# Kernel optimization log

Hardware: AMD Instinct MI355X
Metric: run time of the kernel (lower is better)

The kernel has to match this reference:

```python
import jax, jax.numpy as jnp
import numpy as np

N_SP = 32  # number of superpixels, hardcoded in the original module


def setup_inputs() -> dict:
    key = jax.random.key(0)
    k1, k2 = jax.random.split(key)
    b, c, h, w = 16, 64, 512, 512
    features = jax.random.normal(k1, (b, c, h, w), dtype=jnp.float32)
    superpixel_indices = jax.random.randint(k2, (b, h, w), 0, N_SP, dtype=jnp.int32)
    return {"features": features, "superpixel_indices": superpixel_indices}


def reference(features, superpixel_indices):
    b, c, h, w = features.shape
    # [b, h*w, c]
    feats = jnp.transpose(features, (0, 2, 3, 1)).reshape(b * h * w, c)
    # offset segment ids so all batches reduce in one segment_sum pass
    ids = (superpixel_indices.reshape(b, h * w)
           + (jnp.arange(b, dtype=superpixel_indices.dtype)[:, None] * N_SP)).reshape(-1)
    sums = jax.ops.segment_sum(feats, ids, num_segments=b * N_SP)          # [b*N, c]
    counts = jax.ops.segment_sum(jnp.ones((b * h * w,), feats.dtype), ids,
                                 num_segments=b * N_SP)                     # [b*N]
    # mean per superpixel; empty superpixels stay zero (matches torch init)
    sp = jnp.where(counts[:, None] > 0,
                   sums / jnp.maximum(counts[:, None], 1.0),
                   0.0).reshape(b, N_SP, c)
    # pairwise: sim[i,j] = 1 - 0.5 * ||sp_i - sp_j||^2  (N=32, tiny)
    diff = sp[:, :, None, :] - sp[:, None, :, :]        # [b, N, N, c]
    sim = 1.0 - 0.5 * jnp.sum(diff * diff, axis=-1)     # [b, N, N]
    return sp, sim
```

## Files before the change

### kernel.cpp

```cpp
#include <hip/hip_runtime.h>

#define NSP 32
#define BB  16
#define CC  64
#define HW  (512 * 512)

#define BLOCK  128
#define CHUNK  4096
#define NCHUNK (HW / CHUNK)
#define KIT    (CHUNK / 4 / BLOCK)
#define STR    (NSP + 1)
#define NGRP   (BLOCK / 32)

#define BAR() asm volatile("s_waitcnt lgkmcnt(0)\n\ts_barrier" ::: "memory")

__global__ __launch_bounds__(BLOCK) void sp_accum(const float* __restrict__ feats,
                                                  const int*   __restrict__ spidx,
                                                  float*       __restrict__ sums  ,
                                                  float*       __restrict__ counts)
{
    __shared__ float2 s_priv[BLOCK][STR];
    __shared__ float2 s_pe[NGRP][NSP];
    __shared__ float2 s_po[NGRP][NSP];

    const int tid  = threadIdx.x;
    const int b    = blockIdx.y;
    const int pix0 = blockIdx.x * CHUNK;
    const int bin  = tid & 31;
    const int grp  = tid >> 5;

    float2* row = s_priv[tid];

    uchar4 uu[KIT];
    {
        const int4* ip = (const int4*)(spidx + (size_t)b * HW + pix0);
#pragma unroll
        for (int k = 0; k < KIT; ++k) {
            int4 v = ip[k * BLOCK + tid];
            uu[k] = make_uchar4((unsigned char)(v.x & 31), (unsigned char)(v.y & 31),
                                (unsigned char)(v.z & 31), (unsigned char)(v.w & 31));
        }
    }
#pragma unroll
    for (int s = 0; s < STR; ++s) row[s] = make_float2(0.f, 0.f);

    const float* fb = feats + (size_t)b * CC * HW + pix0;
    float4 pre[KIT][2];
#pragma unroll
    for (int k = 0; k < KIT; ++k) {
        pre[k][0] = ((const float4*)fb)[k * BLOCK + tid];
        pre[k][1] = ((const float4*)(fb + (size_t)HW))[k * BLOCK + tid];
    }

#pragma unroll
    for (int k = 0; k < KIT; ++k) {
        row[uu[k].x].x += 1.f;
        row[uu[k].y].x += 1.f;
        row[uu[k].z].x += 1.f;
        row[uu[k].w].x += 1.f;
    }
    BAR();
    {
        float a = 0.f;
#pragma unroll
        for (int m = 0; m < BLOCK / NGRP; ++m) a += s_priv[grp + m * NGRP][bin].x;
        s_pe[grp][bin].x = a;
    }
    BAR();
#pragma unroll
    for (int s = 0; s < STR; ++s) row[s] = make_float2(0.f, 0.f);
    if (tid < NSP) {
        float r = 0.f;
#pragma unroll
        for (int g = 0; g < NGRP; ++g) r += s_pe[g][tid].x;
        atomicAdd(&counts[b * NSP + tid], r);
    }

    for (int p = 0; p < CC / 2; ++p) {
        const int ch0 = 2 * p;
        float2 (*part)[NSP] = (p & 1) ? s_po : s_pe;

#pragma unroll
        for (int k = 0; k < KIT; ++k) {
            const uchar4 u = uu[k];
            const float4 a = pre[k][0], c = pre[k][1];
            float2 t;
            t = row[u.x]; t.x += a.x; t.y += c.x; row[u.x] = t;
            t = row[u.y]; t.x += a.y; t.y += c.y; row[u.y] = t;
            t = row[u.z]; t.x += a.z; t.y += c.z; row[u.z] = t;
            t = row[u.w]; t.x += a.w; t.y += c.w; row[u.w] = t;
        }
        if (p + 1 < CC / 2) {
            const float* g0 = fb + (size_t)(ch0 + 2) * HW;
#pragma unroll
            for (int k = 0; k < KIT; ++k) {
                pre[k][0] = ((const float4*)g0)[k * BLOCK + tid];
                pre[k][1] = ((const float4*)(g0 + (size_t)HW))[k * BLOCK + tid];
            }
        }
        BAR();
        {
            float2 acc = make_float2(0.f, 0.f);
#pragma unroll
            for (int m = 0; m < BLOCK / NGRP; ++m) {
                float2 v = s_priv[grp + m * NGRP][bin];
                acc.x += v.x; acc.y += v.y;
            }
            part[grp][bin] = acc;
        }
        BAR();
#pragma unroll
        for (int s = 0; s < STR; ++s) row[s] = make_float2(0.f, 0.f);
        if (tid < NSP) {
            float2 r = part[0][tid];
#pragma unroll
            for (int g = 1; g < NGRP; ++g) { r.x += part[g][tid].x; r.y += part[g][tid].y; }
            atomicAdd(&sums[((size_t)b * CC + ch0)     * NSP + tid], r.x);
            atomicAdd(&sums[((size_t)b * CC + ch0 + 1) * NSP + tid], r.y);
        }
    }
}

__global__ __launch_bounds__(256) void sp_finalize(const float* __restrict__ sums,
                                                   const float* __restrict__ counts,
                                                   float*       __restrict__ out)
{
    __shared__ float s_sp[NSP][CC + 1];
    const int b   = blockIdx.x;
    const int tid = threadIdx.x;

    for (int i = tid; i < NSP * CC; i += 256) {
        int sp = i >> 6, c = i & 63;
        float cnt = counts[b * NSP + sp];
        float s   = sums[((size_t)b * CC + c) * NSP + sp];
        float v   = (cnt > 0.0f) ? (s / cnt) : 0.0f;
        s_sp[sp][c] = v;
        out[(size_t)b * NSP * CC + (size_t)sp * CC + c] = v;
    }
    __syncthreads();

    for (int p = tid; p < NSP * NSP; p += 256) {
        int i = p >> 5, j = p & 31;
        float acc = 0.0f;
#pragma unroll
        for (int c = 0; c < CC; ++c) {
            float d = s_sp[i][c] - s_sp[j][c];
            acc = fmaf(d, d, acc);
        }
        out[(size_t)BB * NSP * CC + (size_t)b * NSP * NSP + p] = 1.0f - 0.5f * acc;
    }
}

extern "C" void kernel_launch(void* const* d_in, const int* in_sizes, int n_in,
                              void* d_out, int out_size, void* d_ws, size_t ws_size,
                              hipStream_t stream)
{
    const float* feats = (const float*)d_in[0];
    const int*   spidx = (const int*)d_in[1];
    float*       out   = (float*)d_out;

    float* sums   = (float*)d_ws;
    float* counts = sums + (size_t)BB * CC * NSP;

    hipMemsetAsync(d_ws, 0, ((size_t)BB * CC * NSP + (size_t)BB * NSP) * sizeof(float), stream);

    dim3 g1(NCHUNK, BB);
    sp_accum<<<g1, BLOCK, 0, stream>>>(feats, spidx, sums, counts);

    sp_finalize<<<BB, 256, 0, stream>>>(sums, counts, out);
}
```

Measured before the change: 220.5 us.

## Replace block-wide barrier reductions with per-wavefront histogram reductions and atomics

Each 64-lane wavefront now reduces the private shared-memory histograms of its own lanes. Each lane handles one bin of one channel plane and issues its own atomicAdd. This removes the two block barriers and the cross-group partial buffers on every channel pair. Block size and chunk size are doubled, so the grid is halved while per-thread work stays the same. In exchange there are more global atomics per block and a larger shared-memory footprint, which may limit occupancy.

```diff
diff --git a/kernel.cpp b/kernel.cpp
--- a/kernel.cpp
+++ b/kernel.cpp
@@ -5,31 +5,28 @@
 #define CC  64
 #define HW  (512 * 512)
 
-#define BLOCK  128
-#define CHUNK  4096
+#define BLOCK  256
+#define CHUNK  8192
 #define NCHUNK (HW / CHUNK)
 #define KIT    (CHUNK / 4 / BLOCK)
-#define STR    (NSP + 1)
-#define NGRP   (BLOCK / 32)
-
-#define BAR() asm volatile("s_waitcnt lgkmcnt(0)\n\ts_barrier" ::: "memory")
+#define STR2   66
 
 __global__ __launch_bounds__(BLOCK) void sp_accum(const float* __restrict__ feats,
                                                   const int*   __restrict__ spidx,
                                                   float*       __restrict__ sums  ,
                                                   float*       __restrict__ counts)
 {
-    __shared__ float2 s_priv[BLOCK][STR];
-    __shared__ float2 s_pe[NGRP][NSP];
-    __shared__ float2 s_po[NGRP][NSP];
+    __shared__ float s_priv[BLOCK][STR2];
 
-    const int tid  = threadIdx.x;
-    const int b    = blockIdx.y;
-    const int pix0 = blockIdx.x * CHUNK;
-    const int bin  = tid & 31;
-    const int grp  = tid >> 5;
+    const int tid   = threadIdx.x;
+    const int b     = blockIdx.y;
+    const int pix0  = blockIdx.x * CHUNK;
+    const int lane  = tid & 63;
+    const int wbase = tid & ~63;
+    const int bin   = lane & 31;
+    const int plane = lane >> 5;
 
-    float2* row = s_priv[tid];
+    float2* row = (float2*)&s_priv[tid][0];
 
     uchar4 uu[KIT];
     {
@@ -42,7 +39,7 @@
         }
     }
 #pragma unroll
-    for (int s = 0; s < STR; ++s) row[s] = make_float2(0.f, 0.f);
+    for (int s = 0; s < 33; ++s) row[s] = make_float2(0.f, 0.f);
 
     const float* fb = feats + (size_t)b * CC * HW + pix0;
     float4 pre[KIT][2];
@@ -59,26 +56,20 @@
         row[uu[k].z].x += 1.f;
         row[uu[k].w].x += 1.f;
     }
-    BAR();
     {
-        float a = 0.f;
+        float p0 = 0.f, p1 = 0.f;
 #pragma unroll
-        for (int m = 0; m < BLOCK / NGRP; ++m) a += s_priv[grp + m * NGRP][bin].x;
-        s_pe[grp][bin].x = a;
+        for (int r = 0; r < 64; r += 2) {
+            p0 += s_priv[wbase + r][2 * bin + plane];
+            p1 += s_priv[wbase + r + 1][2 * bin + plane];
+        }
+        atomicAdd(&counts[b * NSP + bin], p0 + p1);
     }
-    BAR();
 #pragma unroll
-    for (int s = 0; s < STR; ++s) row[s] = make_float2(0.f, 0.f);
-    if (tid < NSP) {
-        float r = 0.f;
-#pragma unroll
-        for (int g = 0; g < NGRP; ++g) r += s_pe[g][tid].x;
-        atomicAdd(&counts[b * NSP + tid], r);
-    }
+    for (int s = 0; s < 33; ++s) row[s] = make_float2(0.f, 0.f);
 
     for (int p = 0; p < CC / 2; ++p) {
         const int ch0 = 2 * p;
-        float2 (*part)[NSP] = (p & 1) ? s_po : s_pe;
 
 #pragma unroll
         for (int k = 0; k < KIT; ++k) {
@@ -98,26 +89,15 @@
                 pre[k][1] = ((const float4*)(g0 + (size_t)HW))[k * BLOCK + tid];
             }
         }
-        BAR();
-        {
-            float2 acc = make_float2(0.f, 0.f);
+        float p0 = 0.f, p1 = 0.f;
 #pragma unroll
-            for (int m = 0; m < BLOCK / NGRP; ++m) {
-                float2 v = s_priv[grp + m * NGRP][bin];
-                acc.x += v.x; acc.y += v.y;
-            }
-            part[grp][bin] = acc;
+        for (int r = 0; r < 64; r += 2) {
+            p0 += s_priv[wbase + r][2 * bin + plane];
+            p1 += s_priv[wbase + r + 1][2 * bin + plane];
         }
-        BAR();
+        atomicAdd(&sums[((size_t)b * CC + ch0 + plane) * NSP + bin], p0 + p1);
 #pragma unroll
-        for (int s = 0; s < STR; ++s) row[s] = make_float2(0.f, 0.f);
-        if (tid < NSP) {
-            float2 r = part[0][tid];
-#pragma unroll
-            for (int g = 1; g < NGRP; ++g) { r.x += part[g][tid].x; r.y += part[g][tid].y; }
-            atomicAdd(&sums[((size_t)b * CC + ch0)     * NSP + tid], r.x);
-            atomicAdd(&sums[((size_t)b * CC + ch0 + 1) * NSP + tid], r.y);
-        }
+        for (int s = 0; s < 33; ++s) row[s] = make_float2(0.f, 0.f);
     }
 }
 
```

New measurement: 236.3 us. 1.07x slower.
